# Kernel optimization log

Measured on AMD Instinct MI355X. Metric: run time of the kernel, lower is better.

Reference implementation:

```python
import jax, jax.numpy as jnp
import numpy as np

B, N, D_IN, D_OUT, R = 8, 2048, 256, 256, 4


def setup_inputs() -> dict:
    key = jax.random.key(0)
    k1, k2, k3, k4 = jax.random.split(key, 4)
    x = jax.random.normal(k1, (B, N, D_IN), dtype=jnp.float32)
    adj = jnp.zeros((1,), dtype=jnp.float32)  # unused by the module
    # relation-type matrix: 0 = no edge, 1..R = relation id
    relation = jax.random.randint(k2, (B, N, N), 0, R + 1, dtype=jnp.int32)
    weight = jax.random.normal(k3, (R, D_IN, D_OUT), dtype=jnp.float32) * 0.05
    bias = jax.random.normal(k4, (D_OUT,), dtype=jnp.float32) * 0.05
    return {"x": x, "adj": adj, "relation": relation, "weight": weight, "bias": bias}


def reference(x, adj, relation, weight, bias):
    # Binary per-relation adjacency masks: [R, B, N, N]
    rel_ids = jnp.arange(1, weight.shape[0] + 1, dtype=relation.dtype)
    masks = (relation[None] == rel_ids[:, None, None, None]).astype(x.dtype)
    # Aggregate neighbors per relation: h[r] = A_r @ x  -> [R, B, N, D_in]
    h = jnp.einsum('rbnm,bmd->rbnd', masks, x)
    # Per-relation output transform, summed over relations: [B, N, D_out]
    y = jnp.einsum('rbnd,rdo->bno', h, weight)
    return y + bias
```

## Files before the change

### kernel.cpp

```cpp
#include <hip/hip_runtime.h>
#include <hip/hip_bf16.h>
#include <stdint.h>

typedef uint32_t u32;
typedef uint64_t u64;
typedef __bf16 bf16x8 __attribute__((ext_vector_type(8)));
typedef float f32x4 __attribute__((ext_vector_type(4)));
typedef u32 u32x4 __attribute__((ext_vector_type(4)));

#define NB 8
#define NN 2048
#define DIN 256
#define DOUT 256
#define NR 4
#define KTOT (NN * NR)

#define XW_BYTES   (NB * DOUT * KTOT * 2)
#define PART_BYTES (NB * NN * DOUT * 4)

__device__ __forceinline__ ushort f2bf(float f) {
  union { float f; u32 u; } c; c.f = f;
  return (ushort)((c.u + 0x7FFFu + ((c.u >> 16) & 1u)) >> 16);
}

__device__ __forceinline__ void gload_lds16(const void* g, void* l) {
  __builtin_amdgcn_global_load_lds(
      (const __attribute__((address_space(1))) u32*)g,
      (__attribute__((address_space(3))) u32*)l, 16, 0, 0);
}

__global__ void k0_wT(const float* __restrict__ w, ushort* __restrict__ wT) {
  int i = blockIdx.x * 256 + threadIdx.x;
  int o = i & 255, d = (i >> 8) & 255, r = i >> 16;
  wT[(r * DOUT + o) * DIN + d] = f2bf(w[i]);
}

__global__ __launch_bounds__(512) void k1_xw(const float* __restrict__ x,
                                             const ushort* __restrict__ wT,
                                             ushort* __restrict__ xwT) {
  __shared__ char smem[65536];
  ushort* As = (ushort*)smem;
  ushort* Bs = (ushort*)(smem + 4096);
  const int t = threadIdx.x, l = t & 63, w = t >> 6;
  const int r = w >> 1, oh = w & 1;
  const int blk = blockIdx.x;
  const int b = blk >> 6, rest = blk & 63, mc = rest >> 1, ot = rest & 1;

  f32x4 acc[4][4] = {};
  const int arow = t >> 3, adc = (t & 7) << 2;
  const float* xg = x + ((size_t)(b * NN + mc * 64 + arow) * DIN + adc);

  for (int s = 0; s < 8; ++s) {
    const int d0 = s * 32;
    float4 xv = *(const float4*)(xg + d0);
    ushort4 a4;
    a4.x = f2bf(xv.x); a4.y = f2bf(xv.y); a4.z = f2bf(xv.z); a4.w = f2bf(xv.w);
    *(ushort4*)(As + arow * 32 + adc) = a4;
#pragma unroll
    for (int i = 0; i < 4; ++i) {
      int off = i * 4096 + t * 8;
      int rr = off >> 12, rem = off & 4095, o = rem >> 5, dd = rem & 31;
      const ushort* src = wT + ((size_t)(rr * DOUT + ot * 128 + o) * DIN + d0 + dd);
      gload_lds16(src, Bs + off);
    }
    __syncthreads();
    bf16x8 af[4];
#pragma unroll
    for (int fm = 0; fm < 4; ++fm)
      af[fm] = *(const bf16x8*)(As + (fm * 16 + (l & 15)) * 32 + (l >> 4) * 8);
#pragma unroll
    for (int fo = 0; fo < 4; ++fo) {
      bf16x8 bf = *(const bf16x8*)(Bs + (size_t)(r * 128 + oh * 64 + fo * 16 + (l & 15)) * 32 + (l >> 4) * 8);
#pragma unroll
      for (int fm = 0; fm < 4; ++fm)
        acc[fm][fo] = __builtin_amdgcn_mfma_f32_16x16x32_bf16(af[fm], bf, acc[fm][fo], 0, 0, 0);
    }
    __syncthreads();
  }
  ushort* Cs = (ushort*)smem;
#pragma unroll
  for (int fm = 0; fm < 4; ++fm)
#pragma unroll
    for (int fo = 0; fo < 4; ++fo)
#pragma unroll
      for (int j = 0; j < 4; ++j) {
        int o_loc = oh * 64 + fo * 16 + (l & 15);
        int ml = fm * 16 + (l >> 4) * 4 + j;
        Cs[o_loc * 256 + ml * 4 + r] = f2bf(acc[fm][fo][j]);
      }
  __syncthreads();
#pragma unroll
  for (int i = 0; i < 8; ++i) {
    int el = (i * 512 + t) * 8;
    int o_loc = el >> 8, kp = el & 255;
    *(uint4*)(xwT + (size_t)(b * DOUT + ot * 128 + o_loc) * KTOT + mc * 256 + kp) =
        *(const uint4*)(Cs + el);
  }
}

__global__ __launch_bounds__(256, 2) void k2_main(const int* __restrict__ rel,
                                                  const ushort* __restrict__ xwT,
                                                  float* __restrict__ out,
                                                  float* __restrict__ part) {
  __shared__ char smem[81920];
  const int t = threadIdx.x, l = t & 63, w = t >> 6;
  const int wr = w >> 1, wc = w & 1;
  const int logical = (blockIdx.x & 7) * 64 + (blockIdx.x >> 3);
  const int b = logical >> 6;
  const int nt = (logical >> 2) & 15;
  const int ks = (logical >> 1) & 1;
  const int ot = logical & 1;

  f32x4 acc[4][4] = {};
  const int arow = t >> 1, half = t & 1;
  const int* relg = rel + ((size_t)(b * NN + nt * 128 + arow) * NN + ks * 1024 + half * 8);
  const ushort* xwb = xwT + (size_t)(b * DOUT + ot * 128) * KTOT + ks * 4096;

  char* const Ab0 = smem;
  char* const Ab1 = smem + 16384;
  char* const Bb0 = smem + 32768;
  char* const Bb1 = smem + 49152;
  char* const Bb2 = smem + 65536;

  const int brow = t >> 3;
  const int kd = (((t & 7) ^ ((t >> 3) & 7)) << 3);
  const int aswz = (arow & 7) << 4;
  const int fr = l & 15, fq = l >> 4;
  const int rswz = (fr & 7) << 4;

  int4 rsA0, rsB0, rsA1, rsB1;

#define STAGE_B(S, BBASE)                                                      \
  {                                                                            \
    _Pragma("unroll") for (int i = 0; i < 4; ++i)                              \
      gload_lds16(xwb + (size_t)(brow + 32 * i) * KTOT + (S) * 64 + kd,        \
                  (BBASE) + i * 4096 + t * 16);                                \
  }

#define RELLOAD(S, RA, RB)                                                     \
  RA = *(const int4*)(relg + (S) * 16);                                        \
  RB = *(const int4*)(relg + (S) * 16 + 4);

#define EXPAND_A(ABASE, V0, V1)                                                \
  {                                                                            \
    char* rowp = (ABASE) + arow * 128;                                         \
    int vv[8] = {V0.x, V0.y, V0.z, V0.w, V1.x, V1.y, V1.z, V1.w};              \
    _Pragma("unroll") for (int p = 0; p < 4; ++p) {                            \
      int va = vv[2 * p], vb = vv[2 * p + 1];                                  \
      u32 sa = ((u32)(va - 1) & 3u) * 16u;                                     \
      u32 sb = ((u32)(vb - 1) & 3u) * 16u;                                     \
      u64 ha = va ? (0x3F80ull << sa) : 0ull;                                  \
      u64 hb = vb ? (0x3F80ull << sb) : 0ull;                                  \
      u32x4 e = {(u32)ha, (u32)(ha >> 32), (u32)hb, (u32)(hb >> 32)};          \
      *(u32x4*)(rowp + ((half * 64 + p * 16) ^ aswz)) = e;                     \
    }                                                                          \
  }

#define BARV6()                                                                \
  asm volatile("s_waitcnt vmcnt(6) lgkmcnt(0)" ::: "memory");                  \
  __builtin_amdgcn_s_barrier();                                                \
  __builtin_amdgcn_sched_barrier(0);

#define BARV0()                                                                \
  asm volatile("s_waitcnt vmcnt(0) lgkmcnt(0)" ::: "memory");                  \
  __builtin_amdgcn_s_barrier();                                                \
  __builtin_amdgcn_sched_barrier(0);

#define MFMA_STEP(AC, BC)                                                      \
  __builtin_amdgcn_s_setprio(1);                                               \
  _Pragma("unroll") for (int kk = 0; kk < 2; ++kk) {                           \
    bf16x8 af[4], bfv[4];                                                      \
    const int colb = (kk * 64 + fq * 16) ^ rswz;                               \
    _Pragma("unroll") for (int fm = 0; fm < 4; ++fm)                           \
      af[fm] = *(const bf16x8*)((AC) + (wr * 64 + fm * 16 + fr) * 128 + colb); \
    _Pragma("unroll") for (int fo = 0; fo < 4; ++fo)                           \
      bfv[fo] = *(const bf16x8*)((BC) + (wc * 64 + fo * 16 + fr) * 128 + colb);\
    _Pragma("unroll") for (int fm = 0; fm < 4; ++fm)                           \
      _Pragma("unroll") for (int fo = 0; fo < 4; ++fo)                         \
        acc[fm][fo] = __builtin_amdgcn_mfma_f32_16x16x32_bf16(                 \
            af[fm], bfv[fo], acc[fm][fo], 0, 0, 0);                            \
  }                                                                            \
  __builtin_amdgcn_s_setprio(0);

#define BODY(S, ACUR, BCUR, ANXT, RLA, RLB, RCA, RCB, BSTG)                    \
  {                                                                            \
    STAGE_B((S) + 2, BSTG);                                                    \
    RELLOAD((S) + 2, RLA, RLB);                                                \
    MFMA_STEP(ACUR, BCUR);                                                     \
    EXPAND_A(ANXT, RCA, RCB);                                                  \
    BARV6();                                                                   \
  }

  STAGE_B(0, Bb0);
  RELLOAD(0, rsA0, rsB0);
  STAGE_B(1, Bb1);
  RELLOAD(1, rsA1, rsB1);
  EXPAND_A(Ab0, rsA0, rsB0);
  BARV6();

  for (int s = 0; s < 60; s += 6) {
    BODY(s + 0, Ab0, Bb0, Ab1, rsA0, rsB0, rsA1, rsB1, Bb2);
    BODY(s + 1, Ab1, Bb1, Ab0, rsA1, rsB1, rsA0, rsB0, Bb0);
    BODY(s + 2, Ab0, Bb2, Ab1, rsA0, rsB0, rsA1, rsB1, Bb1);
    BODY(s + 3, Ab1, Bb0, Ab0, rsA1, rsB1, rsA0, rsB0, Bb2);
    BODY(s + 4, Ab0, Bb1, Ab1, rsA0, rsB0, rsA1, rsB1, Bb0);
    BODY(s + 5, Ab1, Bb2, Ab0, rsA1, rsB1, rsA0, rsB0, Bb1);
  }
  BODY(60, Ab0, Bb0, Ab1, rsA0, rsB0, rsA1, rsB1, Bb2);
  BODY(61, Ab1, Bb1, Ab0, rsA1, rsB1, rsA0, rsB0, Bb0);
  {
    MFMA_STEP(Ab0, Bb2);
    EXPAND_A(Ab1, rsA1, rsB1);
    BARV0();
  }
  {
    MFMA_STEP(Ab1, Bb0);
  }

  float* dst = ks ? part : out;
#pragma unroll
  for (int fm = 0; fm < 4; ++fm)
#pragma unroll
    for (int fo = 0; fo < 4; ++fo) {
      int n = nt * 128 + wr * 64 + fm * 16 + fq * 4;
      int o = ot * 128 + wc * 64 + fo * 16 + fr;
#pragma unroll
      for (int j = 0; j < 4; ++j)
        dst[(size_t)(b * NN + n + j) * DOUT + o] = acc[fm][fo][j];
    }
#undef BODY
#undef MFMA_STEP
#undef BARV6
#undef BARV0
#undef EXPAND_A
#undef RELLOAD
#undef STAGE_B
}

__global__ void k3_add(float* __restrict__ out, const float* __restrict__ part,
                       const float* __restrict__ bias) {
  int i = blockIdx.x * 256 + threadIdx.x;
  float4 o = ((const float4*)out)[i];
  float4 p = ((const float4*)part)[i];
  float4 bv = ((const float4*)bias)[i & 63];
  float4 rr;
  rr.x = o.x + p.x + bv.x;
  rr.y = o.y + p.y + bv.y;
  rr.z = o.z + p.z + bv.z;
  rr.w = o.w + p.w + bv.w;
  ((float4*)out)[i] = rr;
}

extern "C" void kernel_launch(void* const* d_in, const int* in_sizes, int n_in,
                              void* d_out, int out_size, void* d_ws, size_t ws_size,
                              hipStream_t stream) {
  const float* x = (const float*)d_in[0];
  const int* rel = (const int*)d_in[2];
  const float* wgt = (const float*)d_in[3];
  const float* bias = (const float*)d_in[4];
  float* out = (float*)d_out;
  char* ws = (char*)d_ws;

  ushort* xwT = (ushort*)ws;
  float* part = (float*)(ws + XW_BYTES);
  ushort* wT = (ushort*)(ws + XW_BYTES + PART_BYTES);

  k0_wT<<<1024, 256, 0, stream>>>(wgt, wT);
  k1_xw<<<512, 512, 0, stream>>>(x, wT, xwT);
  k2_main<<<512, 256, 0, stream>>>(rel, xwT, out, part);
  k3_add<<<4096, 256, 0, stream>>>(out, part, bias);
}
```

Baseline: 118.0 us.

## Load B fragments straight from global into registers, bypassing LDS staging

The precomputed xW operand is no longer staged into LDS with triple buffering. Each wave now loads its own bf16 MFMA B fragments directly from global memory into double-buffered registers, one step ahead. LDS drops from 80KB to 32KB, and the barriers no longer wait on vector-memory counts. In exchange, waves that share a column tile load the same B data twice, each load is a less coalesced 16-byte-per-lane access, the prefetch distance shrinks from two steps to one, and register pressure grows by 64 VGPRs.

```diff
diff --git a/kernel.cpp b/kernel.cpp
--- a/kernel.cpp
+++ b/kernel.cpp
@@ -102,7 +102,7 @@
                                                   const ushort* __restrict__ xwT,
                                                   float* __restrict__ out,
                                                   float* __restrict__ part) {
-  __shared__ char smem[81920];
+  __shared__ char smem[32768];
   const int t = threadIdx.x, l = t & 63, w = t >> 6;
   const int wr = w >> 1, wc = w & 1;
   const int logical = (blockIdx.x & 7) * 64 + (blockIdx.x >> 3);
@@ -114,27 +114,24 @@
   f32x4 acc[4][4] = {};
   const int arow = t >> 1, half = t & 1;
   const int* relg = rel + ((size_t)(b * NN + nt * 128 + arow) * NN + ks * 1024 + half * 8);
-  const ushort* xwb = xwT + (size_t)(b * DOUT + ot * 128) * KTOT + ks * 4096;
 
   char* const Ab0 = smem;
   char* const Ab1 = smem + 16384;
-  char* const Bb0 = smem + 32768;
-  char* const Bb1 = smem + 49152;
-  char* const Bb2 = smem + 65536;
-
-  const int brow = t >> 3;
-  const int kd = (((t & 7) ^ ((t >> 3) & 7)) << 3);
+
   const int aswz = (arow & 7) << 4;
   const int fr = l & 15, fq = l >> 4;
   const int rswz = (fr & 7) << 4;
 
+  const ushort* xwp = xwT + (size_t)(b * DOUT + ot * 128 + wc * 64 + fr) * KTOT +
+                      ks * 4096 + fq * 8;
+
+  bf16x8 bv0[8], bv1[8];
   int4 rsA0, rsB0, rsA1, rsB1;
 
-#define STAGE_B(S, BBASE)                                                      \
-  {                                                                            \
-    _Pragma("unroll") for (int i = 0; i < 4; ++i)                              \
-      gload_lds16(xwb + (size_t)(brow + 32 * i) * KTOT + (S) * 64 + kd,        \
-                  (BBASE) + i * 4096 + t * 16);                                \
+#define LOADB(BV, S)                                                           \
+  _Pragma("unroll") for (int ff = 0; ff < 8; ++ff) {                           \
+    const int fo_ = ff & 3, kk_ = ff >> 2;                                     \
+    BV[ff] = *(const bf16x8*)(xwp + (size_t)fo_ * 16 * KTOT + (S) * 64 + kk_ * 32); \
   }
 
 #define RELLOAD(S, RA, RB)                                                     \
@@ -156,65 +153,52 @@
     }                                                                          \
   }
 
-#define BARV6()                                                                \
-  asm volatile("s_waitcnt vmcnt(6) lgkmcnt(0)" ::: "memory");                  \
+#define BAR()                                                                  \
+  asm volatile("s_waitcnt lgkmcnt(0)" ::: "memory");                           \
   __builtin_amdgcn_s_barrier();                                                \
   __builtin_amdgcn_sched_barrier(0);
 
-#define BARV0()                                                                \
-  asm volatile("s_waitcnt vmcnt(0) lgkmcnt(0)" ::: "memory");                  \
-  __builtin_amdgcn_s_barrier();                                                \
-  __builtin_amdgcn_sched_barrier(0);
-
-#define MFMA_STEP(AC, BC)                                                      \
+#define MFMA_STEP(AC, BV)                                                      \
   __builtin_amdgcn_s_setprio(1);                                               \
   _Pragma("unroll") for (int kk = 0; kk < 2; ++kk) {                           \
-    bf16x8 af[4], bfv[4];                                                      \
+    bf16x8 af[4];                                                              \
     const int colb = (kk * 64 + fq * 16) ^ rswz;                               \
     _Pragma("unroll") for (int fm = 0; fm < 4; ++fm)                           \
       af[fm] = *(const bf16x8*)((AC) + (wr * 64 + fm * 16 + fr) * 128 + colb); \
-    _Pragma("unroll") for (int fo = 0; fo < 4; ++fo)                           \
-      bfv[fo] = *(const bf16x8*)((BC) + (wc * 64 + fo * 16 + fr) * 128 + colb);\
     _Pragma("unroll") for (int fm = 0; fm < 4; ++fm)                           \
       _Pragma("unroll") for (int fo = 0; fo < 4; ++fo)                         \
         acc[fm][fo] = __builtin_amdgcn_mfma_f32_16x16x32_bf16(                 \
-            af[fm], bfv[fo], acc[fm][fo], 0, 0, 0);                            \
+            af[fm], BV[kk * 4 + fo], acc[fm][fo], 0, 0, 0);                    \
   }                                                                            \
   __builtin_amdgcn_s_setprio(0);
 
-#define BODY(S, ACUR, BCUR, ANXT, RLA, RLB, RCA, RCB, BSTG)                    \
+#define BODY(S, P, Q)                                                          \
   {                                                                            \
-    STAGE_B((S) + 2, BSTG);                                                    \
-    RELLOAD((S) + 2, RLA, RLB);                                                \
-    MFMA_STEP(ACUR, BCUR);                                                     \
-    EXPAND_A(ANXT, RCA, RCB);                                                  \
-    BARV6();                                                                   \
-  }
-
-  STAGE_B(0, Bb0);
+    LOADB(bv##Q, (S) + 1);                                                     \
+    RELLOAD((S) + 2, rsA##P, rsB##P);                                          \
+    MFMA_STEP(Ab##P, bv##P);                                                   \
+    EXPAND_A(Ab##Q, rsA##Q, rsB##Q);                                           \
+    BAR();                                                                     \
+  }
+
   RELLOAD(0, rsA0, rsB0);
-  STAGE_B(1, Bb1);
   RELLOAD(1, rsA1, rsB1);
+  LOADB(bv0, 0);
   EXPAND_A(Ab0, rsA0, rsB0);
-  BARV6();
-
-  for (int s = 0; s < 60; s += 6) {
-    BODY(s + 0, Ab0, Bb0, Ab1, rsA0, rsB0, rsA1, rsB1, Bb2);
-    BODY(s + 1, Ab1, Bb1, Ab0, rsA1, rsB1, rsA0, rsB0, Bb0);
-    BODY(s + 2, Ab0, Bb2, Ab1, rsA0, rsB0, rsA1, rsB1, Bb1);
-    BODY(s + 3, Ab1, Bb0, Ab0, rsA1, rsB1, rsA0, rsB0, Bb2);
-    BODY(s + 4, Ab0, Bb1, Ab1, rsA0, rsB0, rsA1, rsB1, Bb0);
-    BODY(s + 5, Ab1, Bb2, Ab0, rsA1, rsB1, rsA0, rsB0, Bb1);
-  }
-  BODY(60, Ab0, Bb0, Ab1, rsA0, rsB0, rsA1, rsB1, Bb2);
-  BODY(61, Ab1, Bb1, Ab0, rsA1, rsB1, rsA0, rsB0, Bb0);
+  BAR();
+
+  for (int s = 0; s < 62; s += 2) {
+    BODY(s, 0, 1);
+    BODY(s + 1, 1, 0);
+  }
   {
-    MFMA_STEP(Ab0, Bb2);
+    LOADB(bv1, 63);
+    MFMA_STEP(Ab0, bv0);
     EXPAND_A(Ab1, rsA1, rsB1);
-    BARV0();
+    BAR();
   }
   {
-    MFMA_STEP(Ab1, Bb0);
+    MFMA_STEP(Ab1, bv1);
   }
 
   float* dst = ks ? part : out;
@@ -230,11 +214,10 @@
     }
 #undef BODY
 #undef MFMA_STEP
-#undef BARV6
-#undef BARV0
+#undef BAR
 #undef EXPAND_A
 #undef RELLOAD
-#undef STAGE_B
+#undef LOADB
 }
 
 __global__ void k3_add(float* __restrict__ out, const float* __restrict__ part,
```

New measurement: 179.8 us. 52.3% more time.

## Build one-hot A fragments in registers instead of staging through LDS

Applied to the files above, without the earlier changes.

The relation-mask A operand is no longer expanded into shared memory. Each lane loads the relation ids it needs directly into registers and builds the bf16 one-hot MFMA fragment on the fly. This drops the LDS A buffers, their writes and reads, and cuts shared memory from 80KB to 48KB, which may allow more blocks per CU. In exchange the relation loads become 8-byte strided gathers per lane rather than coalesced 16-byte row loads, more VMEM instructions are in flight (wait counts adjusted), register pressure rises, and the one-hot construction is now repeated by each wave that shares the same rows.

```diff
diff --git a/kernel.cpp b/kernel.cpp
--- a/kernel.cpp
+++ b/kernel.cpp
@@ -27,6 +27,16 @@
   __builtin_amdgcn_global_load_lds(
       (const __attribute__((address_space(1))) u32*)g,
       (__attribute__((address_space(3))) u32*)l, 16, 0, 0);
+}
+
+__device__ __forceinline__ bf16x8 onehot8(int v0, int v1) {
+  u32 sa = ((u32)(v0 - 1) & 3u) * 16u;
+  u32 sb = ((u32)(v1 - 1) & 3u) * 16u;
+  u64 ha = v0 ? (0x3F80ull << sa) : 0ull;
+  u64 hb = v1 ? (0x3F80ull << sb) : 0ull;
+  union { u32x4 u; bf16x8 b; } c;
+  c.u = (u32x4){(u32)ha, (u32)(ha >> 32), (u32)hb, (u32)(hb >> 32)};
+  return c.b;
 }
 
 __global__ void k0_wT(const float* __restrict__ w, ushort* __restrict__ wT) {
@@ -102,7 +112,7 @@
                                                   const ushort* __restrict__ xwT,
                                                   float* __restrict__ out,
                                                   float* __restrict__ part) {
-  __shared__ char smem[81920];
+  __shared__ char smem[49152];
   const int t = threadIdx.x, l = t & 63, w = t >> 6;
   const int wr = w >> 1, wc = w & 1;
   const int logical = (blockIdx.x & 7) * 64 + (blockIdx.x >> 3);
@@ -112,23 +122,22 @@
   const int ot = logical & 1;
 
   f32x4 acc[4][4] = {};
-  const int arow = t >> 1, half = t & 1;
-  const int* relg = rel + ((size_t)(b * NN + nt * 128 + arow) * NN + ks * 1024 + half * 8);
+  const int fr = l & 15, fq = l >> 4;
+  const int rswz = (fr & 7) << 4;
+
+  const int* relp = rel + ((size_t)(b * NN + nt * 128 + wr * 64 + fr)) * NN +
+                    ks * 1024 + fq * 2;
+
   const ushort* xwb = xwT + (size_t)(b * DOUT + ot * 128) * KTOT + ks * 4096;
 
-  char* const Ab0 = smem;
-  char* const Ab1 = smem + 16384;
-  char* const Bb0 = smem + 32768;
-  char* const Bb1 = smem + 49152;
-  char* const Bb2 = smem + 65536;
+  char* const Bb0 = smem;
+  char* const Bb1 = smem + 16384;
+  char* const Bb2 = smem + 32768;
 
   const int brow = t >> 3;
   const int kd = (((t & 7) ^ ((t >> 3) & 7)) << 3);
-  const int aswz = (arow & 7) << 4;
-  const int fr = l & 15, fq = l >> 4;
-  const int rswz = (fr & 7) << 4;
-
-  int4 rsA0, rsB0, rsA1, rsB1;
+
+  int2 rv0[8], rv1[8];
 
 #define STAGE_B(S, BBASE)                                                      \
   {                                                                            \
@@ -137,84 +146,68 @@
                   (BBASE) + i * 4096 + t * 16);                                \
   }
 
-#define RELLOAD(S, RA, RB)                                                     \
-  RA = *(const int4*)(relg + (S) * 16);                                        \
-  RB = *(const int4*)(relg + (S) * 16 + 4);
-
-#define EXPAND_A(ABASE, V0, V1)                                                \
-  {                                                                            \
-    char* rowp = (ABASE) + arow * 128;                                         \
-    int vv[8] = {V0.x, V0.y, V0.z, V0.w, V1.x, V1.y, V1.z, V1.w};              \
-    _Pragma("unroll") for (int p = 0; p < 4; ++p) {                            \
-      int va = vv[2 * p], vb = vv[2 * p + 1];                                  \
-      u32 sa = ((u32)(va - 1) & 3u) * 16u;                                     \
-      u32 sb = ((u32)(vb - 1) & 3u) * 16u;                                     \
-      u64 ha = va ? (0x3F80ull << sa) : 0ull;                                  \
-      u64 hb = vb ? (0x3F80ull << sb) : 0ull;                                  \
-      u32x4 e = {(u32)ha, (u32)(ha >> 32), (u32)hb, (u32)(hb >> 32)};          \
-      *(u32x4*)(rowp + ((half * 64 + p * 16) ^ aswz)) = e;                     \
-    }                                                                          \
-  }
-
-#define BARV6()                                                                \
-  asm volatile("s_waitcnt vmcnt(6) lgkmcnt(0)" ::: "memory");                  \
+#define RELLOAD(S, RV)                                                         \
+  _Pragma("unroll") for (int ff = 0; ff < 8; ++ff) {                           \
+    const int fm_ = ff >> 1, kk_ = ff & 1;                                     \
+    RV[ff] = *(const int2*)(relp + (size_t)fm_ * 16 * NN + (S) * 16 + kk_ * 8);\
+  }
+
+#define BARV12()                                                               \
+  asm volatile("s_waitcnt vmcnt(12) lgkmcnt(0)" ::: "memory");                 \
   __builtin_amdgcn_s_barrier();                                                \
   __builtin_amdgcn_sched_barrier(0);
 
-#define BARV0()                                                                \
-  asm volatile("s_waitcnt vmcnt(0) lgkmcnt(0)" ::: "memory");                  \
+#define BARV8()                                                                \
+  asm volatile("s_waitcnt vmcnt(8) lgkmcnt(0)" ::: "memory");                  \
   __builtin_amdgcn_s_barrier();                                                \
   __builtin_amdgcn_sched_barrier(0);
 
-#define MFMA_STEP(AC, BC)                                                      \
+#define MFMA_STEP(BC, RV)                                                      \
   __builtin_amdgcn_s_setprio(1);                                               \
   _Pragma("unroll") for (int kk = 0; kk < 2; ++kk) {                           \
-    bf16x8 af[4], bfv[4];                                                      \
+    bf16x8 bfv[4];                                                             \
     const int colb = (kk * 64 + fq * 16) ^ rswz;                               \
-    _Pragma("unroll") for (int fm = 0; fm < 4; ++fm)                           \
-      af[fm] = *(const bf16x8*)((AC) + (wr * 64 + fm * 16 + fr) * 128 + colb); \
     _Pragma("unroll") for (int fo = 0; fo < 4; ++fo)                           \
       bfv[fo] = *(const bf16x8*)((BC) + (wc * 64 + fo * 16 + fr) * 128 + colb);\
-    _Pragma("unroll") for (int fm = 0; fm < 4; ++fm)                           \
+    _Pragma("unroll") for (int fm = 0; fm < 4; ++fm) {                         \
+      bf16x8 af = onehot8(RV[fm * 2 + kk].x, RV[fm * 2 + kk].y);               \
       _Pragma("unroll") for (int fo = 0; fo < 4; ++fo)                         \
         acc[fm][fo] = __builtin_amdgcn_mfma_f32_16x16x32_bf16(                 \
-            af[fm], bfv[fo], acc[fm][fo], 0, 0, 0);                            \
+            af, bfv[fo], acc[fm][fo], 0, 0, 0);                                \
+    }                                                                          \
   }                                                                            \
   __builtin_amdgcn_s_setprio(0);
 
-#define BODY(S, ACUR, BCUR, ANXT, RLA, RLB, RCA, RCB, BSTG)                    \
+#define BODY(S, P, Q, BCUR, BSTG)                                              \
   {                                                                            \
     STAGE_B((S) + 2, BSTG);                                                    \
-    RELLOAD((S) + 2, RLA, RLB);                                                \
-    MFMA_STEP(ACUR, BCUR);                                                     \
-    EXPAND_A(ANXT, RCA, RCB);                                                  \
-    BARV6();                                                                   \
+    RELLOAD((S) + 1, rv##Q);                                                   \
+    MFMA_STEP(BCUR, rv##P);                                                    \
+    BARV12();                                                                  \
   }
 
   STAGE_B(0, Bb0);
-  RELLOAD(0, rsA0, rsB0);
   STAGE_B(1, Bb1);
-  RELLOAD(1, rsA1, rsB1);
-  EXPAND_A(Ab0, rsA0, rsB0);
-  BARV6();
+  RELLOAD(0, rv0);
+  BARV12();
 
   for (int s = 0; s < 60; s += 6) {
-    BODY(s + 0, Ab0, Bb0, Ab1, rsA0, rsB0, rsA1, rsB1, Bb2);
-    BODY(s + 1, Ab1, Bb1, Ab0, rsA1, rsB1, rsA0, rsB0, Bb0);
-    BODY(s + 2, Ab0, Bb2, Ab1, rsA0, rsB0, rsA1, rsB1, Bb1);
-    BODY(s + 3, Ab1, Bb0, Ab0, rsA1, rsB1, rsA0, rsB0, Bb2);
-    BODY(s + 4, Ab0, Bb1, Ab1, rsA0, rsB0, rsA1, rsB1, Bb0);
-    BODY(s + 5, Ab1, Bb2, Ab0, rsA1, rsB1, rsA0, rsB0, Bb1);
-  }
-  BODY(60, Ab0, Bb0, Ab1, rsA0, rsB0, rsA1, rsB1, Bb2);
-  BODY(61, Ab1, Bb1, Ab0, rsA1, rsB1, rsA0, rsB0, Bb0);
+    BODY(s + 0, 0, 1, Bb0, Bb2);
+    BODY(s + 1, 1, 0, Bb1, Bb0);
+    BODY(s + 2, 0, 1, Bb2, Bb1);
+    BODY(s + 3, 1, 0, Bb0, Bb2);
+    BODY(s + 4, 0, 1, Bb1, Bb0);
+    BODY(s + 5, 1, 0, Bb2, Bb1);
+  }
+  BODY(60, 0, 1, Bb0, Bb2);
+  BODY(61, 1, 0, Bb1, Bb0);
   {
-    MFMA_STEP(Ab0, Bb2);
-    EXPAND_A(Ab1, rsA1, rsB1);
-    BARV0();
+    RELLOAD(63, rv1);
+    MFMA_STEP(Bb2, rv0);
+    BARV8();
   }
   {
-    MFMA_STEP(Ab1, Bb0);
+    MFMA_STEP(Bb0, rv1);
   }
 
   float* dst = ks ? part : out;
@@ -230,9 +223,8 @@
     }
 #undef BODY
 #undef MFMA_STEP
-#undef BARV6
-#undef BARV0
-#undef EXPAND_A
+#undef BARV12
+#undef BARV8
 #undef RELLOAD
 #undef STAGE_B
 }
```

After: 189.1 us. 1.6x slower.

## Add 256x256 tile main GEMM with 4-way split-K and phased MFMA schedule

Applied to the files above, without the earlier changes.

Adds a large-tile variant of the main kernel: 512-thread blocks each compute a 256x256 output tile (all of D_OUT) over a quarter of K. The relation matrix is therefore read and expanded once instead of twice per output-column half. It uses double-buffered A/B LDS tiles and a four-phase MFMA schedule with barriers interleaving loads. The split-K partial sums go to three partial buffers that a wider add kernel reduces. This costs more workspace and partial-sum traffic, and falls back to the old path when the workspace is too small.

```diff
diff --git a/kernel.cpp b/kernel.cpp
--- a/kernel.cpp
+++ b/kernel.cpp
@@ -17,6 +17,8 @@
 
 #define XW_BYTES   (NB * DOUT * KTOT * 2)
 #define PART_BYTES (NB * NN * DOUT * 4)
+#define WT_BYTES   (NR * DIN * DOUT * 2)
+#define PART_F     (NB * NN * DOUT)
 
 __device__ __forceinline__ ushort f2bf(float f) {
   union { float f; u32 u; } c; c.f = f;
@@ -98,44 +100,42 @@
   }
 }
 
-__global__ __launch_bounds__(256, 2) void k2_main(const int* __restrict__ rel,
-                                                  const ushort* __restrict__ xwT,
-                                                  float* __restrict__ out,
-                                                  float* __restrict__ part) {
-  __shared__ char smem[81920];
+__global__ __launch_bounds__(512, 2) void k2_big(const int* __restrict__ rel,
+                                                 const ushort* __restrict__ xwT,
+                                                 float* __restrict__ out,
+                                                 float* __restrict__ part) {
+  __shared__ char smem[131072];
   const int t = threadIdx.x, l = t & 63, w = t >> 6;
-  const int wr = w >> 1, wc = w & 1;
-  const int logical = (blockIdx.x & 7) * 64 + (blockIdx.x >> 3);
-  const int b = logical >> 6;
-  const int nt = (logical >> 2) & 15;
-  const int ks = (logical >> 1) & 1;
-  const int ot = logical & 1;
-
-  f32x4 acc[4][4] = {};
+  const int wm = w >> 2, wn = w & 3;
+  const int logical = (blockIdx.x & 7) * 32 + (blockIdx.x >> 3);
+  const int b = logical >> 5;
+  const int nt = (logical >> 2) & 7;
+  const int ks = logical & 3;
+
+  f32x4 acc[8][4] = {};
+  const int fr = l & 15, fq = l >> 4;
+  const int rswz = (fr & 7) << 4;
+
+  char* const Ab0 = smem;
+  char* const Ab1 = smem + 32768;
+  char* const Bb0 = smem + 65536;
+  char* const Bb1 = smem + 98304;
+
   const int arow = t >> 1, half = t & 1;
-  const int* relg = rel + ((size_t)(b * NN + nt * 128 + arow) * NN + ks * 1024 + half * 8);
-  const ushort* xwb = xwT + (size_t)(b * DOUT + ot * 128) * KTOT + ks * 4096;
-
-  char* const Ab0 = smem;
-  char* const Ab1 = smem + 16384;
-  char* const Bb0 = smem + 32768;
-  char* const Bb1 = smem + 49152;
-  char* const Bb2 = smem + 65536;
+  const int aswz = (arow & 7) << 4;
+  const int* relg = rel + ((size_t)(b * NN + nt * 256 + arow)) * NN + ks * 512 + half * 8;
 
   const int brow = t >> 3;
   const int kd = (((t & 7) ^ ((t >> 3) & 7)) << 3);
-  const int aswz = (arow & 7) << 4;
-  const int fr = l & 15, fq = l >> 4;
-  const int rswz = (fr & 7) << 4;
-
-  int4 rsA0, rsB0, rsA1, rsB1;
-
-#define STAGE_B(S, BBASE)                                                      \
-  {                                                                            \
-    _Pragma("unroll") for (int i = 0; i < 4; ++i)                              \
-      gload_lds16(xwb + (size_t)(brow + 32 * i) * KTOT + (S) * 64 + kd,        \
-                  (BBASE) + i * 4096 + t * 16);                                \
-  }
+  const ushort* xwb = xwT + (size_t)b * DOUT * KTOT + ks * 2048;
+
+  int4 rs0a, rs0b, rs1a, rs1b;
+
+#define GLD2(S, BB, I0, I1)                                                    \
+  gload_lds16(xwb + (size_t)(brow + 64 * I0) * KTOT + (S) * 64 + kd,           \
+              (BB) + I0 * 8192 + t * 16);                                      \
+  gload_lds16(xwb + (size_t)(brow + 64 * I1) * KTOT + (S) * 64 + kd,           \
+              (BB) + I1 * 8192 + t * 16);
 
 #define RELLOAD(S, RA, RB)                                                     \
   RA = *(const int4*)(relg + (S) * 16);                                        \
@@ -156,16 +156,189 @@
     }                                                                          \
   }
 
+#define RD_B(BFV, BB)                                                          \
+  _Pragma("unroll") for (int kk = 0; kk < 2; ++kk)                             \
+    _Pragma("unroll") for (int fo = 0; fo < 4; ++fo)                           \
+      BFV[kk * 4 + fo] = *(const bf16x8*)((BB) + (wn * 64 + fo * 16 + fr) * 128 + \
+                                          ((kk * 64 + fq * 16) ^ rswz));
+
+#define RD_A2(A0, A1, A2, A3, AB, FMa, FMb)                                    \
+  A0 = *(const bf16x8*)((AB) + (wm * 128 + FMa * 16 + fr) * 128 + ((fq * 16) ^ rswz)); \
+  A1 = *(const bf16x8*)((AB) + (wm * 128 + FMa * 16 + fr) * 128 + ((64 + fq * 16) ^ rswz)); \
+  A2 = *(const bf16x8*)((AB) + (wm * 128 + FMb * 16 + fr) * 128 + ((fq * 16) ^ rswz)); \
+  A3 = *(const bf16x8*)((AB) + (wm * 128 + FMb * 16 + fr) * 128 + ((64 + fq * 16) ^ rswz));
+
+#define MFMA_Q(A0, A1, A2, A3, BFV, FMa, FMb)                                  \
+  _Pragma("unroll") for (int fo = 0; fo < 4; ++fo)                             \
+    acc[FMa][fo] = __builtin_amdgcn_mfma_f32_16x16x32_bf16(A0, BFV[fo], acc[FMa][fo], 0, 0, 0); \
+  _Pragma("unroll") for (int fo = 0; fo < 4; ++fo)                             \
+    acc[FMa][fo] = __builtin_amdgcn_mfma_f32_16x16x32_bf16(A1, BFV[4 + fo], acc[FMa][fo], 0, 0, 0); \
+  _Pragma("unroll") for (int fo = 0; fo < 4; ++fo)                             \
+    acc[FMb][fo] = __builtin_amdgcn_mfma_f32_16x16x32_bf16(A2, BFV[fo], acc[FMb][fo], 0, 0, 0); \
+  _Pragma("unroll") for (int fo = 0; fo < 4; ++fo)                             \
+    acc[FMb][fo] = __builtin_amdgcn_mfma_f32_16x16x32_bf16(A3, BFV[4 + fo], acc[FMb][fo], 0, 0, 0);
+
+#define PH_MID()                                                               \
+  __builtin_amdgcn_s_barrier();                                                \
+  asm volatile("s_waitcnt lgkmcnt(0)" ::: "memory");                           \
+  __builtin_amdgcn_sched_barrier(0);                                           \
+  __builtin_amdgcn_s_setprio(1)
+
+#define PH_END()                                                               \
+  __builtin_amdgcn_s_setprio(0);                                               \
+  __builtin_amdgcn_s_barrier()
+
+#define STEP(S, P, Q, STG, REL, EXP, VMS)                                      \
+  {                                                                            \
+    bf16x8 bfv[8], af0, af1, af2, af3;                                         \
+                                                                       \
+    RD_B(bfv, Bb##P);                                                          \
+    RD_A2(af0, af1, af2, af3, Ab##P, 0, 1);                                    \
+    if (STG) { GLD2((S) + 1, Bb##Q, 0, 1); }                                   \
+    PH_MID();                                                                  \
+    MFMA_Q(af0, af1, af2, af3, bfv, 0, 1);                                     \
+    PH_END();                                                                  \
+                                                                       \
+    RD_A2(af0, af1, af2, af3, Ab##P, 2, 3);                                    \
+    if (STG) { GLD2((S) + 1, Bb##Q, 2, 3); }                                   \
+    PH_MID();                                                                  \
+    MFMA_Q(af0, af1, af2, af3, bfv, 2, 3);                                     \
+    PH_END();                                                                  \
+     \
+    RD_A2(af0, af1, af2, af3, Ab##P, 4, 5);                                    \
+    if (EXP) { EXPAND_A(Ab##Q, rs##Q##a, rs##Q##b); }                          \
+    if (REL) { RELLOAD((S) + 2, rs##P##a, rs##P##b); }                         \
+    PH_MID();                                                                  \
+    MFMA_Q(af0, af1, af2, af3, bfv, 4, 5);                                     \
+    PH_END();                                                                  \
+                                                                       \
+    RD_A2(af0, af1, af2, af3, Ab##P, 6, 7);                                    \
+    PH_MID();                                                                  \
+    MFMA_Q(af0, af1, af2, af3, bfv, 6, 7);                                     \
+    __builtin_amdgcn_s_setprio(0);                                             \
+    asm volatile("s_waitcnt vmcnt(" VMS ")" ::: "memory");                     \
+    __builtin_amdgcn_s_barrier();                                              \
+    __builtin_amdgcn_sched_barrier(0);                                         \
+  }
+
+  GLD2(0, Bb0, 0, 1);
+  GLD2(0, Bb0, 2, 3);
+  RELLOAD(0, rs0a, rs0b);
+  RELLOAD(1, rs1a, rs1b);
+  EXPAND_A(Ab0, rs0a, rs0b);
+  asm volatile("s_waitcnt lgkmcnt(0)" ::: "memory");
+  __builtin_amdgcn_s_barrier();
+  __builtin_amdgcn_sched_barrier(0);
+
+  for (int s = 0; s < 30; s += 2) {
+    STEP(s, 0, 1, 1, 1, 1, "2");
+    STEP(s + 1, 1, 0, 1, 1, 1, "2");
+  }
+  STEP(30, 0, 1, 1, 0, 1, "0");
+  STEP(31, 1, 0, 0, 0, 0, "63");
+
+  float* dst = (ks == 0) ? out : part + (size_t)(ks - 1) * PART_F;
+#pragma unroll
+  for (int fm = 0; fm < 8; ++fm)
+#pragma unroll
+    for (int fo = 0; fo < 4; ++fo) {
+      int n = nt * 256 + wm * 128 + fm * 16 + fq * 4;
+      int o = wn * 64 + fo * 16 + fr;
+#pragma unroll
+      for (int j = 0; j < 4; ++j)
+        dst[(size_t)(b * NN + n + j) * DOUT + o] = acc[fm][fo][j];
+    }
+#undef STEP
+#undef PH_END
+#undef PH_MID
+#undef MFMA_Q
+#undef RD_A2
+#undef RD_B
+#undef EXPAND_A
+#undef RELLOAD
+#undef GLD2
+}
+
+__global__ void k3_big(float* __restrict__ out, const float* __restrict__ part,
+                       const float* __restrict__ bias) {
+  int i = blockIdx.x * 256 + threadIdx.x;
+  const float4* p = (const float4*)part;
+  float4 o = ((const float4*)out)[i];
+  float4 a = p[i];
+  float4 c = p[i + (PART_F >> 2)];
+  float4 d = p[i + (PART_F >> 1)];
+  float4 bv = ((const float4*)bias)[i & 63];
+  float4 rr;
+  rr.x = o.x + a.x + c.x + d.x + bv.x;
+  rr.y = o.y + a.y + c.y + d.y + bv.y;
+  rr.z = o.z + a.z + c.z + d.z + bv.z;
+  rr.w = o.w + a.w + c.w + d.w + bv.w;
+  ((float4*)out)[i] = rr;
+}
+
+__global__ __launch_bounds__(256, 2) void k2_r4(const int* __restrict__ rel,
+                                                const ushort* __restrict__ xwT,
+                                                float* __restrict__ out,
+                                                float* __restrict__ part) {
+  __shared__ char smem[81920];
+  const int t = threadIdx.x, l = t & 63, w = t >> 6;
+  const int wr = w >> 1, wc = w & 1;
+  const int logical = (blockIdx.x & 7) * 64 + (blockIdx.x >> 3);
+  const int b = logical >> 6;
+  const int nt = (logical >> 2) & 15;
+  const int ks = (logical >> 1) & 1;
+  const int ot = logical & 1;
+
+  f32x4 acc[4][4] = {};
+  const int arow = t >> 1, half = t & 1;
+  const int* relg = rel + ((size_t)(b * NN + nt * 128 + arow) * NN + ks * 1024 + half * 8);
+  const ushort* xwb = xwT + (size_t)(b * DOUT + ot * 128) * KTOT + ks * 4096;
+
+  char* const Ab0 = smem;
+  char* const Ab1 = smem + 16384;
+  char* const Bb0 = smem + 32768;
+  char* const Bb1 = smem + 49152;
+  char* const Bb2 = smem + 65536;
+
+  const int brow = t >> 3;
+  const int kd = (((t & 7) ^ ((t >> 3) & 7)) << 3);
+  const int aswz = (arow & 7) << 4;
+  const int fr = l & 15, fq = l >> 4;
+  const int rswz = (fr & 7) << 4;
+
+  int4 rsA0, rsB0, rsA1, rsB1;
+
+#define STAGE_B(S, BBASE)                                                      \
+  {                                                                            \
+    _Pragma("unroll") for (int i = 0; i < 4; ++i)                              \
+      gload_lds16(xwb + (size_t)(brow + 32 * i) * KTOT + (S) * 64 + kd,        \
+                  (BBASE) + i * 4096 + t * 16);                                \
+  }
+#define RELLOAD(S, RA, RB)                                                     \
+  RA = *(const int4*)(relg + (S) * 16);                                        \
+  RB = *(const int4*)(relg + (S) * 16 + 4);
+#define EXPAND_A(ABASE, V0, V1)                                                \
+  {                                                                            \
+    char* rowp = (ABASE) + arow * 128;                                         \
+    int vv[8] = {V0.x, V0.y, V0.z, V0.w, V1.x, V1.y, V1.z, V1.w};              \
+    _Pragma("unroll") for (int p = 0; p < 4; ++p) {                            \
+      int va = vv[2 * p], vb = vv[2 * p + 1];                                  \
+      u32 sa = ((u32)(va - 1) & 3u) * 16u;                                     \
+      u32 sb = ((u32)(vb - 1) & 3u) * 16u;                                     \
+      u64 ha = va ? (0x3F80ull << sa) : 0ull;                                  \
+      u64 hb = vb ? (0x3F80ull << sb) : 0ull;                                  \
+      u32x4 e = {(u32)ha, (u32)(ha >> 32), (u32)hb, (u32)(hb >> 32)};          \
+      *(u32x4*)(rowp + ((half * 64 + p * 16) ^ aswz)) = e;                     \
+    }                                                                          \
+  }
 #define BARV6()                                                                \
   asm volatile("s_waitcnt vmcnt(6) lgkmcnt(0)" ::: "memory");                  \
   __builtin_amdgcn_s_barrier();                                                \
   __builtin_amdgcn_sched_barrier(0);
-
 #define BARV0()                                                                \
   asm volatile("s_waitcnt vmcnt(0) lgkmcnt(0)" ::: "memory");                  \
   __builtin_amdgcn_s_barrier();                                                \
   __builtin_amdgcn_sched_barrier(0);
-
 #define MFMA_STEP(AC, BC)                                                      \
   __builtin_amdgcn_s_setprio(1);                                               \
   _Pragma("unroll") for (int kk = 0; kk < 2; ++kk) {                           \
@@ -181,7 +354,6 @@
             af[fm], bfv[fo], acc[fm][fo], 0, 0, 0);                            \
   }                                                                            \
   __builtin_amdgcn_s_setprio(0);
-
 #define BODY(S, ACUR, BCUR, ANXT, RLA, RLB, RCA, RCB, BSTG)                    \
   {                                                                            \
     STAGE_B((S) + 2, BSTG);                                                    \
@@ -237,8 +409,8 @@
 #undef STAGE_B
 }
 
-__global__ void k3_add(float* __restrict__ out, const float* __restrict__ part,
-                       const float* __restrict__ bias) {
+__global__ void k3_r4(float* __restrict__ out, const float* __restrict__ part,
+                      const float* __restrict__ bias) {
   int i = blockIdx.x * 256 + threadIdx.x;
   float4 o = ((const float4*)out)[i];
   float4 p = ((const float4*)part)[i];
@@ -261,12 +433,22 @@
   float* out = (float*)d_out;
   char* ws = (char*)d_ws;
 
-  ushort* xwT = (ushort*)ws;
-  float* part = (float*)(ws + XW_BYTES);
-  ushort* wT = (ushort*)(ws + XW_BYTES + PART_BYTES);
-
-  k0_wT<<<1024, 256, 0, stream>>>(wgt, wT);
-  k1_xw<<<512, 512, 0, stream>>>(x, wT, xwT);
-  k2_main<<<512, 256, 0, stream>>>(rel, xwT, out, part);
-  k3_add<<<4096, 256, 0, stream>>>(out, part, bias);
-}
+  const size_t need_big = (size_t)XW_BYTES + 3ull * PART_BYTES + WT_BYTES;
+  if (ws_size >= need_big) {
+    ushort* xwT = (ushort*)ws;
+    float* part = (float*)(ws + XW_BYTES);
+    ushort* wT = (ushort*)(ws + XW_BYTES + 3ull * PART_BYTES);
+    k0_wT<<<1024, 256, 0, stream>>>(wgt, wT);
+    k1_xw<<<512, 512, 0, stream>>>(x, wT, xwT);
+    k2_big<<<256, 512, 0, stream>>>(rel, xwT, out, part);
+    k3_big<<<4096, 256, 0, stream>>>(out, part, bias);
+  } else {
+    ushort* xwT = (ushort*)ws;
+    float* part = (float*)(ws + XW_BYTES);
+    ushort* wT = (ushort*)(ws + XW_BYTES + PART_BYTES);
+    k0_wT<<<1024, 256, 0, stream>>>(wgt, wT);
+    k1_xw<<<512, 512, 0, stream>>>(x, wT, xwT);
+    k2_r4<<<512, 256, 0, stream>>>(rel, xwT, out, part);
+    k3_r4<<<4096, 256, 0, stream>>>(out, part, bias);
+  }
+}
```

Measured after the change: 120.1 us. About the same (+1.7%).
